# Kernel optimization log

Measured on AMD Instinct MI355X. Metric: run time of the kernel, lower is better.

## Reference

```python
import jax, jax.numpy as jnp
import numpy as np

B, S, HID = 2, 2048, 4096
H, KV, D = 32, 8, 128          # heads, kv heads, head_dim
G = H // KV                    # num_key_value_groups
THETA = 10000.0
SCALE = 1.0 / np.sqrt(D)
NEG_INF = -1e9


def rotate_half(x):
    x1, x2 = x[..., : D // 2], x[..., D // 2 :]
    return jnp.concatenate([-x2, x1], axis=-1)


def rope_tables(seq_len):
    inv_freq = 1.0 / (THETA ** (jnp.arange(0, D, 2, dtype=jnp.float32) / D))
    t = jnp.arange(seq_len, dtype=jnp.float32)
    freqs = jnp.outer(t, inv_freq)              # [S, D/2]
    emb = jnp.concatenate([freqs, freqs], -1)   # [S, D]
    return jnp.cos(emb), jnp.sin(emb)


def setup_inputs() -> dict:
    key = jax.random.key(0)
    ks = jax.random.split(key, 5)
    w = 0.02
    x = jax.random.normal(ks[0], (B, S, HID), jnp.float32)
    Wq = jax.random.normal(ks[1], (HID, H * D), jnp.float32) * w
    Wk = jax.random.normal(ks[2], (HID, KV * D), jnp.float32) * w
    Wv = jax.random.normal(ks[3], (HID, KV * D), jnp.float32) * w
    Wo = jax.random.normal(ks[4], (H * D, HID), jnp.float32) * w
    position_ids = jnp.broadcast_to(jnp.arange(S, dtype=jnp.int32), (B, S))
    causal = jnp.where(
        jnp.arange(S)[:, None] >= jnp.arange(S)[None, :], 0.0, NEG_INF
    ).astype(jnp.float32)
    attention_mask = jnp.broadcast_to(causal, (B, 1, S, S))
    return {
        "by_pass_hidden_states": x,
        "attention_mask": attention_mask,
        "position_ids": position_ids,
        "Wq": Wq,
        "Wk": Wk,
        "Wv": Wv,
        "Wo": Wo,
    }


def reference(by_pass_hidden_states, attention_mask, position_ids, Wq, Wk, Wv, Wo):
    x = by_pass_hidden_states
    # QKV projections (weights stored [in, out])
    q = (x @ Wq).reshape(B, S, H, D).transpose(0, 2, 1, 3)    # [B,H,S,D]
    k = (x @ Wk).reshape(B, S, KV, D).transpose(0, 2, 1, 3)   # [B,KV,S,D]
    v = (x @ Wv).reshape(B, S, KV, D).transpose(0, 2, 1, 3)   # [B,KV,S,D]
    # RoPE
    cos_t, sin_t = rope_tables(S)
    cos = cos_t[position_ids][:, None]   # [B,1,S,D]
    sin = sin_t[position_ids][:, None]
    q = q * cos + rotate_half(q) * sin
    k = k * cos + rotate_half(k) * sin
    # GQA attention without materializing repeated K/V: group query heads
    qg = q.reshape(B, KV, G, S, D)
    scores = jnp.einsum("bkgsd,bktd->bkgst", qg, k) * SCALE   # [B,KV,G,S,S]
    scores = scores.reshape(B, H, S, S) + attention_mask
    probs = jax.nn.softmax(scores.astype(jnp.float32), axis=-1).astype(x.dtype)
    ctx = jnp.einsum("bkgst,bktd->bkgsd", probs.reshape(B, KV, G, S, S), v)
    ctx = ctx.reshape(B, H, S, D).transpose(0, 2, 1, 3).reshape(B, S, H * D)
    return ctx @ Wo
```

## Files before the change

kernel.cpp:

```cpp
#include <hip/hip_runtime.h>
#include <cstdint>
#include <cstddef>

#define B_   2
#define S_   2048
#define HID_ 4096
#define H_   32
#define KV_  8
#define D_   128
#define M_   (B_*S_)
#define QSTR 6144

typedef __attribute__((ext_vector_type(8))) short bf16x8;
typedef __attribute__((ext_vector_type(4))) float f32x4;
typedef __attribute__((ext_vector_type(16))) float f32x16;
typedef __attribute__((ext_vector_type(4))) unsigned int u32x4;
typedef unsigned short u16;
typedef unsigned int   u32;

#define KSC (0.08838834764831845f * 1.4426950408889634f)

__device__ __forceinline__ float bf2f(u16 v){ u32 u = ((u32)v) << 16; return __builtin_bit_cast(float, u); }
__device__ __forceinline__ u16 f2bf(float f){
  u32 u = __builtin_bit_cast(u32, f);
  u32 r = u + 0x7fffu + ((u >> 16) & 1u);
  return (u16)(r >> 16);
}

__device__ __forceinline__ void gload_lds16(const void* g, void* lds){
  __builtin_amdgcn_global_load_lds(
      (const __attribute__((address_space(1))) void*)g,
      (__attribute__((address_space(3))) void*)lds, 16, 0, 0);
}

__global__ void cast_f32_bf16(const float* __restrict__ in, u16* __restrict__ out, int n){
  int i = (blockIdx.x * blockDim.x + threadIdx.x) * 4;
  if (i >= n) return;
  float4 v = *(const float4*)(in + i);
  ushort4 o;
  o.x = f2bf(v.x); o.y = f2bf(v.y); o.z = f2bf(v.z); o.w = f2bf(v.w);
  *(ushort4*)(out + i) = o;
}

__global__ __launch_bounds__(256) void tcast(const float* __restrict__ W, u16* __restrict__ WT,
                                             int Kd, int Nd){
  __shared__ __align__(16) u16 t[64][65];
  int k0 = blockIdx.x * 64, n0 = blockIdx.y * 64;
  int lx = threadIdx.x & 15, ly = threadIdx.x >> 4;
  #pragma unroll
  for (int rr = 0; rr < 4; ++rr){
    int r = rr * 16 + ly;
    float4 v = *(const float4*)(W + (size_t)(k0 + r) * Nd + n0 + lx * 4);
    t[lx*4+0][r] = f2bf(v.x);
    t[lx*4+1][r] = f2bf(v.y);
    t[lx*4+2][r] = f2bf(v.z);
    t[lx*4+3][r] = f2bf(v.w);
  }
  __syncthreads();
  #pragma unroll
  for (int rr = 0; rr < 4; ++rr){
    int r = rr * 16 + ly;
    ushort4 o;
    o.x = t[r][lx*4+0]; o.y = t[r][lx*4+1]; o.z = t[r][lx*4+2]; o.w = t[r][lx*4+3];
    *(ushort4*)(WT + (size_t)(n0 + r) * Kd + k0 + lx * 4) = o;
  }
}

__global__ __launch_bounds__(256) void vtrans(const u16* __restrict__ QKV, u16* __restrict__ Vt){
  __shared__ __align__(16) u16 t[64][65];
  int stile = blockIdx.x;
  int b = blockIdx.y >> 4, vt = blockIdx.y & 15;
  int s0 = stile * 64, c0 = vt * 64;
  int lx = threadIdx.x & 15, ly = threadIdx.x >> 4;
  #pragma unroll
  for (int rr = 0; rr < 4; ++rr){
    int r = rr * 16 + ly;
    ushort4 v = *(const ushort4*)(QKV + (size_t)(b*S_ + s0 + r) * QSTR + 5120 + c0 + lx*4);
    t[lx*4+0][r]=v.x; t[lx*4+1][r]=v.y; t[lx*4+2][r]=v.z; t[lx*4+3][r]=v.w;
  }
  __syncthreads();
  #pragma unroll
  for (int rr = 0; rr < 4; ++rr){
    int r = rr * 16 + ly;
    ushort4 o;
    o.x=t[r][lx*4+0]; o.y=t[r][lx*4+1]; o.z=t[r][lx*4+2]; o.w=t[r][lx*4+3];
    *(ushort4*)(Vt + (size_t)(b*1024 + c0 + r) * S_ + s0 + lx*4) = o;
  }
}

__global__ void rope_k(u16* __restrict__ X, const int* __restrict__ pos, int hshift, int stride){
  int idx = blockIdx.x * 256 + threadIdx.x;
  int i = idx & 63;
  int h = (idx >> 6) & ((1 << hshift) - 1);
  int t = idx >> (6 + hshift);
  u16* p0 = X + (size_t)t * stride + h * D_ + i;
  float x1 = bf2f(p0[0]), x2 = bf2f(p0[64]);
  float fpos = (float)pos[t];
  float invf = exp2f(-(float)(2 * i) * (13.287712379549449f / 128.0f));
  float f = fpos * invf;
  float sv = __sinf(f), cv = __cosf(f);
  p0[0]  = f2bf(x1 * cv - x2 * sv);
  p0[64] = f2bf(x2 * cv + x1 * sv);
}


#define SBAR() __builtin_amdgcn_sched_barrier(0)
#define BARX() do{ SBAR(); __builtin_amdgcn_s_barrier(); SBAR(); }while(0)

#define STG_A(PB, HALF, KT) do{ \
  gload_lds16(Ag + off0 + (size_t)(HALF)*1048576 + (size_t)(KT)*128, \
              (char*)smem + (PB)*32768 + (HALF)*16384 + w*1024); \
  gload_lds16(Ag + off0 + 524288 + (size_t)(HALF)*1048576 + (size_t)(KT)*128, \
              (char*)smem + (PB)*32768 + (HALF)*16384 + 8192 + w*1024); }while(0)
#define STG_B(PB, HALF, KT) do{ \
  gload_lds16(Bg + off0 + (size_t)(HALF)*1048576 + (size_t)(KT)*128, \
              (char*)smem + 65536 + (PB)*32768 + (HALF)*16384 + w*1024); \
  gload_lds16(Bg + off0 + 524288 + (size_t)(HALF)*1048576 + (size_t)(KT)*128, \
              (char*)smem + 65536 + (PB)*32768 + (HALF)*16384 + 8192 + w*1024); }while(0)

#define RD_A(DST, HALF) do{ \
  _Pragma("unroll") for (int ks = 0; ks < 2; ++ks) \
  _Pragma("unroll") for (int m = 0; m < 4; ++m) \
    DST[ks][m] = *(const bf16x8*)&smem[P*16384 + (HALF)*8192 + aRowBase + m*1024 + csw[ks]]; }while(0)
#define RD_B(DST, HALF) do{ \
  _Pragma("unroll") for (int ks = 0; ks < 2; ++ks) \
  _Pragma("unroll") for (int n = 0; n < 2; ++n) \
    DST[ks][n] = *(const bf16x8*)&smem[32768 + P*16384 + (HALF)*8192 + bRowBase + n*1024 + csw[ks]]; }while(0)

template<int MO, int NO>
__device__ __forceinline__ void mfma_quad(f32x4 (&acc)[8][4],
                                          const bf16x8 (&af)[2][4], const bf16x8 (&bf)[2][2]){
  __builtin_amdgcn_s_setprio(1);
  #pragma unroll
  for (int ks = 0; ks < 2; ++ks)
    #pragma unroll
    for (int m = 0; m < 4; ++m)
      #pragma unroll
      for (int n = 0; n < 2; ++n)
        acc[MO+m][NO+n] = __builtin_amdgcn_mfma_f32_16x16x32_bf16(af[ks][m], bf[ks][n], acc[MO+m][NO+n], 0, 0, 0);
  __builtin_amdgcn_s_setprio(0);
}

template<bool OUTF32>
__global__ __launch_bounds__(512, 2) void gemm256(const u16* __restrict__ A, const u16* __restrict__ Bt,
                                                  void* __restrict__ C, int Nn, int mt){
  __shared__ __align__(16) u16 smem[65536];
  const int tid = threadIdx.x;
  const int l = tid & 63, w = tid >> 6;
  const int lr = l & 15, lk = l >> 4;
  const int wr = w >> 2, wc = w & 3;

  const int nwg = gridDim.x;
  const int sbid = ((int)blockIdx.x & 7) * (nwg >> 3) + ((int)blockIdx.x >> 3);
  const int bx = sbid % mt, by = sbid / mt;
  const size_t arow0 = (size_t)bx * 256;
  const size_t brow0 = (size_t)by * 256;
  const char* Ag = (const char*)(A + arow0 * 4096);
  const char* Bg = (const char*)(Bt + brow0 * 4096);

  const size_t off0 = (size_t)(w * 8 + (l >> 3)) * 8192 + (size_t)(((l & 7) ^ (l >> 3)) << 4);

  const int aRowBase = (wr*64 + lr) * 64;
  const int bRowBase = (wc*32 + lr) * 64;
  int csw[2];
  csw[0] = ((lk     ) ^ (lr & 7)) << 3;
  csw[1] = ((lk + 4) ^ (lr & 7)) << 3;

  f32x4 acc[8][4];
  #pragma unroll
  for (int i = 0; i < 8; ++i)
    #pragma unroll
    for (int j = 0; j < 4; ++j){ acc[i][j][0]=0.f; acc[i][j][1]=0.f; acc[i][j][2]=0.f; acc[i][j][3]=0.f; }

  STG_A(0, 0, 0); STG_B(0, 0, 0); STG_A(0, 1, 0); STG_B(0, 1, 0);
  STG_A(1, 0, 1); STG_B(1, 0, 1); STG_A(1, 1, 1); STG_B(1, 1, 1);
  asm volatile("s_waitcnt vmcnt(8)" ::: "memory");
  BARX();

  for (int t = 0; t < 64; ++t){
    const int P = t & 1;
    bf16x8 a0h[2][4], a1[2][4], b0[2][2], b1[2][2];
    RD_A(a0h, 0); RD_B(b0, 0);
    BARX();
    mfma_quad<0,0>(acc, a0h, b0);
    BARX();
    if (t < 62){ STG_A(P, 0, t+2); STG_B(P, 0, t+2); }
    RD_A(a1, 1);
    BARX();
    mfma_quad<4,0>(acc, a1, b0);
    BARX();
    if (t < 62){ STG_A(P, 1, t+2); }
    RD_B(b1, 1);
    BARX();
    mfma_quad<4,2>(acc, a1, b1);
    BARX();
    if (t < 62){ STG_B(P, 1, t+2); }
    BARX();
    mfma_quad<0,2>(acc, a0h, b1);
    if (t < 62)      asm volatile("s_waitcnt vmcnt(8)" ::: "memory");
    else if (t < 63) asm volatile("s_waitcnt vmcnt(0)" ::: "memory");
    BARX();
  }

  #pragma unroll
  for (int mh = 0; mh < 2; ++mh)
    #pragma unroll
    for (int m = 0; m < 4; ++m)
      #pragma unroll
      for (int nh = 0; nh < 2; ++nh)
        #pragma unroll
        for (int n = 0; n < 2; ++n)
          #pragma unroll
          for (int j = 0; j < 4; ++j){
            size_t gr = arow0 + mh*128 + wr*64 + m*16 + lk*4 + j;
            size_t gc = brow0 + nh*128 + wc*32 + n*16 + lr;
            float v = acc[mh*4+m][nh*2+n][j];
            if (OUTF32) ((float*)C)[gr * Nn + gc] = v;
            else        ((u16*)C)[gr * Nn + gc] = f2bf(v);
          }
}

__global__ __launch_bounds__(512, 2) void attn_k(const u16* __restrict__ QKV,
                                                 const u16* __restrict__ Vtg,
                                                 u16* __restrict__ ctx){
  __shared__ __align__(16) u16 smem[32768];
  const int tid = threadIdx.x;
  const int l = tid & 63, w = tid >> 6;
  const int lane31 = l & 31, hi = l >> 5;
  const int hb = blockIdx.x;
  const int b = hb >> 5, h = hb & 31, kvh = h >> 2;
  const int qb = 7 - blockIdx.y;
  const int q0w = qb * 256 + w * 32;
  const int qg = q0w + lane31;

  const u16* Qp = QKV + (size_t)b * S_ * QSTR + (size_t)h * D_;
  const char* Kp = (const char*)(QKV + (size_t)b * S_ * QSTR + 4096 + (size_t)kvh * D_);
  const char* Vp = (const char*)(Vtg + ((size_t)b * 1024 + kvh * 128) * S_);

  bf16x8 qf[8];
  #pragma unroll
  for (int dt = 0; dt < 8; ++dt)
    qf[dt] = *(const bf16x8*)(Qp + (size_t)qg * QSTR + dt * 16 + hi * 8);

  const int krow0 = (2*w)*4 + (l >> 4), krow1 = krow0 + 4;
  const size_t koff0 = (size_t)krow0 * (QSTR*2) + (((l & 15) << 4) ^ ((krow0 & 7) << 4));
  const size_t koff1 = (size_t)krow1 * (QSTR*2) + (((l & 15) << 4) ^ ((krow1 & 7) << 4));
  const int vrow0 = (2*w)*8 + (l >> 3), vrow1 = vrow0 + 8;
  const size_t voff0 = (size_t)vrow0 * (S_*2) + (((l & 7) << 4) ^ ((vrow0 & 7) << 4));
  const size_t voff1 = (size_t)vrow1 * (S_*2) + (((l & 7) << 4) ^ ((vrow1 & 7) << 4));

  f32x16 acc[4];
  #pragma unroll
  for (int dt = 0; dt < 4; ++dt)
    #pragma unroll
    for (int i = 0; i < 16; ++i) acc[dt][i] = 0.f;
  float mrow = -3e38f, lsum = 0.f;

  const int nt = qb * 4 + 4;

  auto STAGE = [&](int t, int bufn){
    char* Kb = (char*)smem + bufn * 16384;
    char* Vb = (char*)smem + 32768 + bufn * 16384;
    size_t kb = (size_t)t * 64 * (QSTR*2);
    size_t vb = (size_t)t * 128;
    gload_lds16(Kp + kb + koff0, Kb + (2*w)*1024);
    gload_lds16(Kp + kb + koff1, Kb + (2*w+1)*1024);
    gload_lds16(Vp + vb + voff0, Vb + (2*w)*1024);
    gload_lds16(Vp + vb + voff1, Vb + (2*w+1)*1024);
  };

  STAGE(0, 0);
  __syncthreads();
  int buf = 0;
  for (int t = 0; t < nt; ++t){
    if (t + 1 < nt) STAGE(t + 1, buf ^ 1);
    const int kbase = t * 64;
    if (kbase <= q0w + 31){
      const char* Kb = (const char*)smem + buf * 16384;
      const char* Vb = (const char*)smem + 32768 + buf * 16384;
      const int swz = (lane31 & 7) << 4;

      f32x16 s0, s1;
      #pragma unroll
      for (int i = 0; i < 16; ++i){ s0[i] = 0.f; s1[i] = 0.f; }
      #pragma unroll
      for (int dt = 0; dt < 8; ++dt){
        bf16x8 kf = *(const bf16x8*)(Kb + lane31*256 + ((dt*32 + hi*16) ^ swz));
        s0 = __builtin_amdgcn_mfma_f32_32x32x16_bf16(kf, qf[dt], s0, 0, 0, 0);
      }
      #pragma unroll
      for (int dt = 0; dt < 8; ++dt){
        bf16x8 kf = *(const bf16x8*)(Kb + (32 + lane31)*256 + ((dt*32 + hi*16) ^ swz));
        s1 = __builtin_amdgcn_mfma_f32_32x32x16_bf16(kf, qf[dt], s1, 0, 0, 0);
      }

      if (kbase + 63 > q0w){
        int thr = qg - kbase;
        #pragma unroll
        for (int r = 0; r < 16; ++r){
          int kc = (r & 3) + 8*(r >> 2) + 4*hi;
          s0[r] = (kc > thr)      ? -1e30f : s0[r];
          s1[r] = (kc + 32 > thr) ? -1e30f : s1[r];
        }
      }

      float tmax = s0[0];
      #pragma unroll
      for (int r = 1; r < 16; ++r) tmax = fmaxf(tmax, s0[r]);
      #pragma unroll
      for (int r = 0; r < 16; ++r) tmax = fmaxf(tmax, s1[r]);
      tmax = fmaxf(tmax, __shfl_xor(tmax, 32));
      float mn = fmaxf(mrow, tmax);
      float rf = exp2f((mrow - mn) * KSC);
      mrow = mn;
      float ps = 0.f;
      #pragma unroll
      for (int r = 0; r < 16; ++r){
        float a = exp2f((s0[r] - mn) * KSC);
        float c = exp2f((s1[r] - mn) * KSC);
        s0[r] = a; s1[r] = c; ps += a + c;
      }
      ps += __shfl_xor(ps, 32);
      lsum = lsum * rf + ps;
      #pragma unroll
      for (int dt = 0; dt < 4; ++dt)
        #pragma unroll
        for (int i = 0; i < 16; ++i) acc[dt][i] *= rf;

      u32 pw[16];
      #pragma unroll
      for (int g = 0; g < 4; ++g){
        pw[2*g]     = (u32)f2bf(s0[4*g])   | ((u32)f2bf(s0[4*g+1]) << 16);
        pw[2*g+1]   = (u32)f2bf(s0[4*g+2]) | ((u32)f2bf(s0[4*g+3]) << 16);
        pw[8+2*g]   = (u32)f2bf(s1[4*g])   | ((u32)f2bf(s1[4*g+1]) << 16);
        pw[8+2*g+1] = (u32)f2bf(s1[4*g+2]) | ((u32)f2bf(s1[4*g+3]) << 16);
      }

      #pragma unroll
      for (int kt = 0; kt < 4; ++kt){
        u32 W0 = pw[kt*4+0], W1 = pw[kt*4+1], W2 = pw[kt*4+2], W3 = pw[kt*4+3];
        u32 x0 = hi ? W0 : W2;
        u32 x1 = hi ? W1 : W3;
        u32 y0 = __shfl_xor(x0, 32);
        u32 y1 = __shfl_xor(x1, 32);
        u32 w0 = hi ? y0 : W0;
        u32 w1 = hi ? y1 : W1;
        u32 w2 = hi ? W2 : y0;
        u32 w3 = hi ? W3 : y1;
        u32x4 pk; pk[0]=w0; pk[1]=w1; pk[2]=w2; pk[3]=w3;
        bf16x8 pa = __builtin_bit_cast(bf16x8, pk);
        #pragma unroll
        for (int dt = 0; dt < 4; ++dt){
          bf16x8 vf = *(const bf16x8*)(Vb + (dt*32 + lane31)*128 + ((kt*32 + hi*16) ^ swz));
          acc[dt] = __builtin_amdgcn_mfma_f32_32x32x16_bf16(vf, pa, acc[dt], 0, 0, 0);
        }
      }
    }
    __syncthreads();
    buf ^= 1;
  }

  __syncthreads();
  u16* Ot = smem + w * 4096;
  float inv = 1.f / lsum;
  #pragma unroll
  for (int dt = 0; dt < 4; ++dt)
    #pragma unroll
    for (int r = 0; r < 16; ++r){
      int d = dt*32 + (r & 3) + 8*(r >> 2) + 4*hi;
      Ot[lane31*128 + (d ^ ((lane31 & 15) << 2))] = f2bf(acc[dt][r] * inv);
    }
  u16* outp = ctx + ((size_t)(b * S_ + q0w)) * HID_ + h * D_;
  #pragma unroll
  for (int it = 0; it < 16; ++it){
    int id = it * 64 + l;
    int q = id >> 5;
    int c4 = (id & 31) * 4;
    ushort4 vv = *(const ushort4*)(Ot + q*128 + (c4 ^ ((q & 15) << 2)));
    *(ushort4*)(outp + (size_t)q * HID_ + c4) = vv;
  }
}

extern "C" void kernel_launch(void* const* d_in, const int* in_sizes, int n_in,
                              void* d_out, int out_size, void* d_ws, size_t ws_size,
                              hipStream_t stream) {
  const float* x  = (const float*)d_in[0];
  const int*   pos = (const int*)d_in[2];
  const float* Wq = (const float*)d_in[3];
  const float* Wk = (const float*)d_in[4];
  const float* Wv = (const float*)d_in[5];
  const float* Wo = (const float*)d_in[6];

  char* ws = (char*)d_ws;
  u16* xb   = (u16*)(ws);
  u16* WT   = (u16*)(ws + ((size_t)32 << 20));
  u16* WoT  = (u16*)(ws + ((size_t)80 << 20));
  u16* QKVb = (u16*)(ws + ((size_t)112 << 20));
  u16* Vtg  = (u16*)(ws + ((size_t)32 << 20));

  cast_f32_bf16<<<16384, 256, 0, stream>>>(x, xb, HID_ * M_);
  tcast<<<dim3(64, 64), 256, 0, stream>>>(Wq, WT, 4096, 4096);
  tcast<<<dim3(64, 16), 256, 0, stream>>>(Wk, WT + (size_t)4096 * 4096, 4096, 1024);
  tcast<<<dim3(64, 16), 256, 0, stream>>>(Wv, WT + (size_t)5120 * 4096, 4096, 1024);
  tcast<<<dim3(64, 64), 256, 0, stream>>>(Wo, WoT, 4096, 4096);
  gemm256<false><<<16 * 24, 512, 0, stream>>>(xb, WT, QKVb, 6144, 16);
  rope_k<<<32768, 256, 0, stream>>>(QKVb,        pos, 5, QSTR);
  rope_k<<<8192,  256, 0, stream>>>(QKVb + 4096, pos, 3, QSTR);
  vtrans<<<dim3(32, 32), 256, 0, stream>>>(QKVb, Vtg);
  attn_k<<<dim3(64, 8), 512, 0, stream>>>(QKVb, Vtg, xb);
  gemm256<true><<<16 * 16, 512, 0, stream>>>(xb, WoT, d_out, 4096, 16);
}
```

Measured before the change: 546.9 us.

## Prefetch next tile's first-half LDS fragments across GEMM loop iterations

The GEMM main loop is restructured so the first-half A/B fragments for the next k-step are read from LDS at the end of the current iteration, overlapping with the last MFMA block. Second-half reads are moved earlier. The vmcnt wait moves mid-iteration so the next buffer's data is ready before the prefetch. This hides LDS read latency before the first MFMA quad, at the cost of more live registers and a tighter wait schedule.

```diff
diff --git a/kernel.cpp b/kernel.cpp
--- a/kernel.cpp
+++ b/kernel.cpp
@@ -118,14 +118,14 @@
   gload_lds16(Bg + off0 + 524288 + (size_t)(HALF)*1048576 + (size_t)(KT)*128, \
               (char*)smem + 65536 + (PB)*32768 + (HALF)*16384 + 8192 + w*1024); }while(0)
 
-#define RD_A(DST, HALF) do{ \
+#define RD_A(DST, PP, HALF) do{ \
   _Pragma("unroll") for (int ks = 0; ks < 2; ++ks) \
   _Pragma("unroll") for (int m = 0; m < 4; ++m) \
-    DST[ks][m] = *(const bf16x8*)&smem[P*16384 + (HALF)*8192 + aRowBase + m*1024 + csw[ks]]; }while(0)
-#define RD_B(DST, HALF) do{ \
+    DST[ks][m] = *(const bf16x8*)&smem[(PP)*16384 + (HALF)*8192 + aRowBase + m*1024 + csw[ks]]; }while(0)
+#define RD_B(DST, PP, HALF) do{ \
   _Pragma("unroll") for (int ks = 0; ks < 2; ++ks) \
   _Pragma("unroll") for (int n = 0; n < 2; ++n) \
-    DST[ks][n] = *(const bf16x8*)&smem[32768 + P*16384 + (HALF)*8192 + bRowBase + n*1024 + csw[ks]]; }while(0)
+    DST[ks][n] = *(const bf16x8*)&smem[32768 + (PP)*16384 + (HALF)*8192 + bRowBase + n*1024 + csw[ks]]; }while(0)
 
 template<int MO, int NO>
 __device__ __forceinline__ void mfma_quad(f32x4 (&acc)[8][4],
@@ -176,29 +176,34 @@
   STG_A(1, 0, 1); STG_B(1, 0, 1); STG_A(1, 1, 1); STG_B(1, 1, 1);
   asm volatile("s_waitcnt vmcnt(8)" ::: "memory");
   BARX();
+  bf16x8 a0c[2][4], b0c[2][2], a1f[2][4], b1f[2][2];
+  RD_A(a0c, 0, 0); RD_B(b0c, 0, 0);
 
   for (int t = 0; t < 64; ++t){
     const int P = t & 1;
-    bf16x8 a0h[2][4], a1[2][4], b0[2][2], b1[2][2];
-    RD_A(a0h, 0); RD_B(b0, 0);
-    BARX();
-    mfma_quad<0,0>(acc, a0h, b0);
+    RD_A(a1f, P, 1);
+    BARX();
+    mfma_quad<0,0>(acc, a0c, b0c);
     BARX();
     if (t < 62){ STG_A(P, 0, t+2); STG_B(P, 0, t+2); }
-    RD_A(a1, 1);
-    BARX();
-    mfma_quad<4,0>(acc, a1, b0);
-    BARX();
-    if (t < 62){ STG_A(P, 1, t+2); }
-    RD_B(b1, 1);
-    BARX();
-    mfma_quad<4,2>(acc, a1, b1);
+    RD_B(b1f, P, 1);
+    BARX();
+    mfma_quad<4,0>(acc, a1f, b0c);
+    BARX();
+    if (t < 62){
+      STG_A(P, 1, t+2);
+      asm volatile("s_waitcnt vmcnt(6)" ::: "memory");
+    } else if (t == 62){
+      asm volatile("s_waitcnt vmcnt(0)" ::: "memory");
+    }
+    BARX();
+    mfma_quad<4,2>(acc, a1f, b1f);
     BARX();
     if (t < 62){ STG_B(P, 1, t+2); }
     BARX();
-    mfma_quad<0,2>(acc, a0h, b1);
-    if (t < 62)      asm volatile("s_waitcnt vmcnt(8)" ::: "memory");
-    else if (t < 63) asm volatile("s_waitcnt vmcnt(0)" ::: "memory");
+    mfma_quad<0,2>(acc, a0c, b1f);
+    SBAR();
+    if (t < 63){ RD_A(a0c, P^1, 0); RD_B(b0c, P^1, 0); }
     BARX();
   }
 
```

After: 545.1 us. Within noise of the previous version (-0.3%).
